# Optimization experiments

Hardware: AMD Instinct MI355X
Metric: run time of the kernel (lower is better)

Reference implementation:

```python
import jax, jax.numpy as jnp
import numpy as np

N, E = 25000, 400000
NF, EF, HNF, HEF = 32, 32, 128, 128
NOUT, EOUT = 32, 32
D_N, D_E = HNF + NF, HEF + EF  # concat dims fed to the GNN layer


def _glorot(key, shape):
    return jax.random.normal(key, shape, jnp.float32) / np.sqrt(shape[0])


def setup_inputs() -> dict:
    key = jax.random.key(0)
    ks = jax.random.split(key, 10)
    return {
        "nf": jax.random.normal(ks[0], (N, NF), jnp.float32),
        "ef": jax.random.normal(ks[1], (E, EF), jnp.float32),
        "src": jax.random.randint(ks[2], (E,), 0, N),
        "dst": jax.random.randint(ks[3], (E,), 0, N),
        # AttnMPNNLayer params: edge model, attention logit model, node model
        "W_edge": _glorot(ks[4], (2 * D_N + D_E, HEF)),
        "b_edge": jnp.zeros((HEF,), jnp.float32),
        "W_attn": _glorot(ks[5], (2 * D_N + D_E, 1)),
        "b_attn": jnp.zeros((1,), jnp.float32),
        "W_node": _glorot(ks[6], (D_N + HEF, HNF)),
        "b_node": jnp.zeros((HNF,), jnp.float32),
        # output heads (MLP with num_neurons=[] -> single Linear)
        "W_nout": _glorot(ks[7], (HNF, NOUT)),
        "b_nout": jnp.zeros((NOUT,), jnp.float32),
        "W_eout": _glorot(ks[8], (HEF, EOUT)),
        "b_eout": jnp.zeros((EOUT,), jnp.float32),
        "n_iters": 3,
    }


def _attn_mpnn_layer(hnf, hef, src, dst, W_edge, b_edge, W_attn, b_attn, W_node, b_node):
    """Attention message passing: gather endpoints, edge MLP + attn logit,
    edge-softmax over incoming edges (per dst node), scatter-aggregate, node MLP."""
    n = hnf.shape[0]
    e_in = jnp.concatenate([hnf[src], hnf[dst], hef], axis=-1)   # [E, 2*D_N + D_E]
    m = jax.nn.relu(e_in @ W_edge + b_edge)                      # [E, HEF] new edge feats
    logit = (e_in @ W_attn + b_attn)[:, 0]                       # [E]
    # numerically stable edge softmax grouped by destination node
    lmax = jax.ops.segment_max(logit, dst, num_segments=n)
    lmax = jnp.where(jnp.isfinite(lmax), lmax, 0.0)              # isolated nodes -> 0
    a = jnp.exp(logit - lmax[dst])
    denom = jax.ops.segment_sum(a, dst, num_segments=n)
    alpha = a / jnp.maximum(denom[dst], 1e-16)
    agg = jax.ops.segment_sum(alpha[:, None] * m, dst, num_segments=n)  # [N, HEF]
    un = jax.nn.relu(jnp.concatenate([hnf, agg], axis=-1) @ W_node + b_node)  # [N, HNF]
    return un, m


def reference(nf, ef, src, dst, W_edge, b_edge, W_attn, b_attn, W_node, b_node,
              W_nout, b_nout, W_eout, b_eout, n_iters):
    hnf = jnp.zeros((nf.shape[0], HNF), nf.dtype)
    hef = jnp.zeros((ef.shape[0], HEF), ef.dtype)
    for _ in range(n_iters):
        hnf = jnp.concatenate([hnf, nf], axis=-1)   # input re-injection
        hef = jnp.concatenate([hef, ef], axis=-1)
        hnf, hef = _attn_mpnn_layer(hnf, hef, src, dst,
                                    W_edge, b_edge, W_attn, b_attn, W_node, b_node)
    unf = hnf @ W_nout + b_nout
    uef = hef @ W_eout + b_eout
    return unf, uef
```

## Files before the change

### kernel.cpp

```cpp
#include <hip/hip_runtime.h>


#define GN 25000
#define GE 400000
#define NODE_BLKS 196
#define EDGE_BLKS 6250
#define HEAD_EBLKS 3125

typedef unsigned short u16;
typedef __attribute__((ext_vector_type(8))) short bf16x8;
typedef __attribute__((ext_vector_type(4))) float f32x4;

__device__ inline float b2f(u16 v) {
  union { unsigned int u; float f; } x; x.u = ((unsigned int)v) << 16; return x.f;
}
__device__ inline u16 f2b(float f) {
  union { float f; unsigned int u; } x; x.f = f;
  unsigned int u = x.u;
  u += 0x7fffu + ((u >> 16) & 1u);
  return (u16)(u >> 16);
}

__global__ void detect_dtype(const void* nf, int* flag) {
  if (blockIdx.x == 0 && threadIdx.x == 0) {
    const u16* p = (const u16*)nf;
    int cnt = 0;
    for (int i = 0; i < 512; i += 2) {
      int e = (p[i] >> 7) & 0xFF;
      if (e >= 0x70 && e <= 0x85) cnt++;
    }
    *flag = (cnt < 128) ? 1 : 0;
  }
}

__global__ void convert_kernel(const void* src, u16* dst, long n, const int* flag) {
  int f32 = *flag;
  long i = (long)blockIdx.x * blockDim.x + threadIdx.x;
  long stride = (long)gridDim.x * blockDim.x;
  for (; i < n; i += stride)
    dst[i] = f32 ? f2b(((const float*)src)[i]) : ((const u16*)src)[i];
}

__global__ void gather_ef(const void* ef, const int* eid, u16* efc, const int* flag) {
  int f32 = *flag;
  long idx = (long)blockIdx.x * blockDim.x + threadIdx.x;
  long ntot = (long)GE * 4;
  if (idx >= ntot) return;
  long j = idx >> 2;
  int g = (int)(idx & 3) * 8;
  long e = eid[j];
  uint4 out;
  if (f32) {
    const float* pf = (const float*)ef + e * 32 + g;
    float4 a = ((const float4*)pf)[0];
    float4 b = ((const float4*)pf)[1];
    unsigned int* ov = (unsigned int*)&out;
    ov[0] = (unsigned int)f2b(a.x) | ((unsigned int)f2b(a.y) << 16);
    ov[1] = (unsigned int)f2b(a.z) | ((unsigned int)f2b(a.w) << 16);
    ov[2] = (unsigned int)f2b(b.x) | ((unsigned int)f2b(b.y) << 16);
    ov[3] = (unsigned int)f2b(b.z) | ((unsigned int)f2b(b.w) << 16);
  } else {
    out = *(const uint4*)((const u16*)ef + e * 32 + g);
  }
  *(uint4*)(efc + j * 32 + g) = out;
}

__global__ void prep_weights(const void* We, const void* Wn, const void* Wa,
                             const void* Won, const void* Woe,
                             const void* be, const void* ba, const void* bn,
                             const void* bno, const void* beo,
                             u16* WeT, u16* WnpT, u16* WnuT, u16* WoN, u16* WoE,
                             u16* Wac, u16* bec, u16* bac, u16* bnc, u16* bnoc, u16* beoc,
                             const int* flag) {
  int f32 = *flag;
  auto ld = [&](const void* p, long i) -> u16 {
    return f32 ? f2b(((const float*)p)[i]) : ((const u16*)p)[i];
  };
  int tid = blockIdx.x * blockDim.x + threadIdx.x;
  int nt = gridDim.x * blockDim.x;
  for (int i = tid; i < 128 * 160; i += nt) { int n = i / 160, k = i % 160; WeT[i] = ld(We, (long)(320 + k) * 128 + n); }
  for (int i = tid; i < 256 * 160; i += nt) {
    int c = i / 160, k = i % 160;
    WnpT[i] = (c < 128) ? ld(We, (long)k * 128 + c) : ld(We, (long)(160 + k) * 128 + (c - 128));
  }
  for (int i = tid; i < 128 * 288; i += nt) { int c = i / 288, k = i % 288; WnuT[i] = ld(Wn, (long)k * 128 + c); }
  for (int i = tid; i < 32 * 128; i += nt) {
    int c = i / 128, k = i % 128;
    WoN[i] = ld(Won, (long)k * 32 + c);
    WoE[i] = ld(Woe, (long)k * 32 + c);
  }
  for (int i = tid; i < 480; i += nt) Wac[i] = ld(Wa, i);
  for (int i = tid; i < 128; i += nt) { bec[i] = ld(be, i); bnc[i] = ld(bn, i); }
  for (int i = tid; i < 32; i += nt) { bnoc[i] = ld(bno, i); beoc[i] = ld(beo, i); }
  if (tid == 0) bac[0] = ld(ba, 0);
}

__global__ void hist_kernel(const int* dst, int* counts, int n) {
  for (int e = blockIdx.x * blockDim.x + threadIdx.x; e < n; e += gridDim.x * blockDim.x)
    atomicAdd(&counts[dst[e]], 1);
}

__global__ __launch_bounds__(1024) void scan_kernel(int* cursor, int* rowptr, int n) {
  __shared__ int part[1024];
  int t = threadIdx.x;
  int per = (n + 1023) / 1024;
  int lo = t * per;
  int hi = lo + per; if (hi > n) hi = n;
  if (lo > n) lo = n;
  int s = 0;
  for (int i = lo; i < hi; ++i) s += cursor[i];
  part[t] = s;
  __syncthreads();
  for (int off = 1; off < 1024; off <<= 1) {
    int v = (t >= off) ? part[t - off] : 0;
    __syncthreads();
    part[t] += v;
    __syncthreads();
  }
  int run = (t > 0) ? part[t - 1] : 0;
  for (int i = lo; i < hi; ++i) {
    int c = cursor[i];
    cursor[i] = run;
    rowptr[i + 1] = run + c;
    run += c;
  }
  if (t == 0) rowptr[0] = 0;
}

__global__ void fill_kernel(const int* src, const int* dst, int* cursor, int* eid,
                            int* srcs, int* dsts, int n) {
  for (int e = blockIdx.x * blockDim.x + threadIdx.x; e < n; e += gridDim.x * blockDim.x) {
    int d = dst[e];
    int p = atomicAdd(&cursor[d], 1);
    eid[p] = e;
    srcs[p] = src[e];
    dsts[p] = d;
  }
}

__global__ __launch_bounds__(256)
void node_proj(const u16* HNF, const u16* nf, const u16* WnpT, const u16* W_attn,
               u16* Xs, u16* Xd, float* as_, float* ad_, int kc0, int nrows) {
  __shared__ union {
    struct { __align__(16) u16 A[128][40]; __align__(16) u16 B[128][40]; } st;
    u16 C[128][130];
  } sm;
  __shared__ float dotbuf[128][2];
  int sel = blockIdx.y, blk = blockIdx.x, tid = threadIdx.x;
  int lane = tid & 63, wv = tid >> 6, wr = wv & 1, wc = wv >> 1;
  const u16* BT = WnpT + sel * 128 * 160;
  u16* OUT = sel ? Xd : Xs;
  float* AOUT = sel ? ad_ : as_;
  const u16* wa = W_attn + sel * 160;
  f32x4 acc[4][4];
  f32x4 zf = {0.f, 0.f, 0.f, 0.f};
  for (int i = 0; i < 4; ++i) for (int j = 0; j < 4; ++j) acc[i][j] = zf;
  float dp = 0.f;
  int arow = tid >> 1, ahalf = (tid & 1) * 16;
  int r0 = blk * 128;
  int ra = r0 + arow;
  uint4 va0 = make_uint4(0, 0, 0, 0), va1 = make_uint4(0, 0, 0, 0), vb0, vb1;
  {
    if (ra < nrows) {
      const uint4* p = (kc0 < 4) ? (const uint4*)(HNF + (size_t)ra * 128 + kc0 * 32 + ahalf)
                                 : (const uint4*)(nf + (size_t)ra * 32 + ahalf);
      va0 = p[0]; va1 = p[1];
    }
    const uint4* pb = (const uint4*)(BT + arow * 160 + kc0 * 32 + ahalf);
    vb0 = pb[0]; vb1 = pb[1];
  }
  for (int kc = kc0; kc < 5; ++kc) {
    *(uint4*)&sm.st.A[arow][ahalf] = va0;
    *(uint4*)&sm.st.A[arow][ahalf + 8] = va1;
    *(uint4*)&sm.st.B[arow][ahalf] = vb0;
    *(uint4*)&sm.st.B[arow][ahalf + 8] = vb1;
    if (kc < 4) {
      int kn = kc + 1;
      va0 = make_uint4(0, 0, 0, 0); va1 = make_uint4(0, 0, 0, 0);
      if (ra < nrows) {
        const uint4* p = (kn < 4) ? (const uint4*)(HNF + (size_t)ra * 128 + kn * 32 + ahalf)
                                  : (const uint4*)(nf + (size_t)ra * 32 + ahalf);
        va0 = p[0]; va1 = p[1];
      }
      const uint4* pb = (const uint4*)(BT + arow * 160 + kn * 32 + ahalf);
      vb0 = pb[0]; vb1 = pb[1];
    }
    __syncthreads();
    {
      float s = 0.f;
      for (int j = 0; j < 16; ++j) s += b2f(sm.st.A[arow][ahalf + j]) * b2f(wa[kc * 32 + ahalf + j]);
      dp += s;
    }
    int q = lane >> 4, l16 = lane & 15;
    bf16x8 af[4], bfr[4];
    for (int i = 0; i < 4; ++i) af[i] = *(const bf16x8*)&sm.st.A[wr * 64 + i * 16 + l16][q * 8];
    for (int j = 0; j < 4; ++j) bfr[j] = *(const bf16x8*)&sm.st.B[wc * 64 + j * 16 + l16][q * 8];
    for (int i = 0; i < 4; ++i)
      for (int j = 0; j < 4; ++j)
        acc[i][j] = __builtin_amdgcn_mfma_f32_16x16x32_bf16(af[i], bfr[j], acc[i][j], 0, 0, 0);
    __syncthreads();
  }
  dotbuf[arow][tid & 1] = dp;
  {
    int q = lane >> 4, l16 = lane & 15;
    for (int i = 0; i < 4; ++i)
      for (int j = 0; j < 4; ++j) {
        int col = wc * 64 + j * 16 + l16;
        for (int rr = 0; rr < 4; ++rr) {
          int row = wr * 64 + i * 16 + q * 4 + rr;
          sm.C[row][col] = f2b(acc[i][j][rr]);
        }
      }
  }
  __syncthreads();
  if (tid < 128) {
    int r = r0 + tid;
    if (r < nrows) AOUT[r] = dotbuf[tid][0] + dotbuf[tid][1];
  }
  {
    int r = tid >> 1, h = (tid & 1) * 64;
    int rg = r0 + r;
    if (rg < nrows) {
      uint4* po = (uint4*)(OUT + (size_t)rg * 128 + h);
      for (int k = 0; k < 8; ++k) {
        unsigned int a0 = *(const unsigned int*)&sm.C[r][h + k * 8];
        unsigned int a1 = *(const unsigned int*)&sm.C[r][h + k * 8 + 2];
        unsigned int a2 = *(const unsigned int*)&sm.C[r][h + k * 8 + 4];
        unsigned int a3 = *(const unsigned int*)&sm.C[r][h + k * 8 + 6];
        po[k] = make_uint4(a0, a1, a2, a3);
      }
    }
  }
}

template <int KC0>
__global__ __launch_bounds__(256, 4)
void edge_fused(u16* HEF, const u16* ef, const u16* WeT, const u16* W_attn,
                const u16* b_edge, const u16* b_attn, const int* srcs, const int* dsts,
                const u16* Xs, const u16* Xd, const float* as_, const float* ad_,
                float* logit) {
  __shared__ union {
    __align__(16) u16 A[2][64][40];
    float C[64][65];
  } sm;
  __shared__ float dotbuf[64];
  int blk = blockIdx.x, tid = threadIdx.x;
  int lane = tid & 63, wv = tid >> 6, wr = wv & 1, wc = wv >> 1;
  int q = lane >> 4, l16 = lane & 15;
  f32x4 acc[2][4];
  f32x4 zf = {0.f, 0.f, 0.f, 0.f};
  for (int i = 0; i < 2; ++i) for (int j = 0; j < 4; ++j) acc[i][j] = zf;
  float dp[2] = {0.f, 0.f};
  long e0 = (long)blk * 64;
  long ea = e0 + (tid >> 2);
  int qp = (tid & 3) * 8;
  const u16* wa = W_attn + 320;

  uint4 va = (KC0 < 4) ? *(const uint4*)(HEF + ea * 128 + KC0 * 32 + qp)
                       : *(const uint4*)(ef + ea * 32 + qp);
  bf16x8 bfp[2][4];
#pragma unroll
  for (int j = 0; j < 4; ++j)
    bfp[KC0 & 1][j] = *(const bf16x8*)(WeT + (size_t)(wc * 64 + j * 16 + l16) * 160 + KC0 * 32 + q * 8);

#pragma unroll
  for (int kc = KC0; kc < 5; ++kc) {
    int buf = kc & 1;
    *(uint4*)&sm.A[buf][tid >> 2][qp] = va;
    if (kc < 4) {
      va = (kc + 1 < 4) ? *(const uint4*)(HEF + ea * 128 + (kc + 1) * 32 + qp)
                        : *(const uint4*)(ef + ea * 32 + qp);
#pragma unroll
      for (int j = 0; j < 4; ++j)
        bfp[(kc + 1) & 1][j] = *(const bf16x8*)(WeT + (size_t)(wc * 64 + j * 16 + l16) * 160 + (kc + 1) * 32 + q * 8);
    }
    __syncthreads();
    bf16x8 af[2];
    for (int i = 0; i < 2; ++i) af[i] = *(const bf16x8*)&sm.A[buf][wr * 32 + i * 16 + l16][q * 8];
    if (wc == 0) {
      bf16x8 wv8 = *(const bf16x8*)&wa[kc * 32 + q * 8];
      float wf[8];
      for (int j = 0; j < 8; ++j) wf[j] = b2f((u16)wv8[j]);
      for (int i = 0; i < 2; ++i)
        for (int j = 0; j < 8; ++j) dp[i] += b2f((u16)af[i][j]) * wf[j];
    }
    for (int i = 0; i < 2; ++i)
      for (int j = 0; j < 4; ++j)
        acc[i][j] = __builtin_amdgcn_mfma_f32_16x16x32_bf16(af[i], bfp[buf][j], acc[i][j], 0, 0, 0);
  }
  if (wc == 0) {
    for (int i = 0; i < 2; ++i) {
      dp[i] += __shfl_xor(dp[i], 16);
      dp[i] += __shfl_xor(dp[i], 32);
    }
    if (q == 0)
      for (int i = 0; i < 2; ++i) dotbuf[wr * 32 + i * 16 + l16] = dp[i];
  }
  int r = tid >> 2, qh = tid & 3;
  long e = e0 + r;
  int s = srcs[e], d = dsts[e];
#pragma unroll
  for (int p = 0; p < 2; ++p) {
    int cb = p * 64 + qh * 16;
    const uint4* ps = (const uint4*)(Xs + (size_t)s * 128 + cb);
    const uint4* pd = (const uint4*)(Xd + (size_t)d * 128 + cb);
    uint4 gs0 = ps[0], gs1 = ps[1], gd0 = pd[0], gd1 = pd[1];
    __syncthreads();
    if (wc == p) {
      for (int i = 0; i < 2; ++i)
        for (int j = 0; j < 4; ++j) {
          int col = j * 16 + l16;
          float bb = b2f(b_edge[p * 64 + col]);
          for (int rr = 0; rr < 4; ++rr)
            sm.C[wr * 32 + i * 16 + q * 4 + rr][col] = acc[i][j][rr] + bb;
        }
    }
    __syncthreads();
    if (p == 0 && tid < 64) {
      long ee = e0 + tid;
      logit[ee] = dotbuf[tid] + as_[srcs[ee]] + ad_[dsts[ee]] + b2f(b_attn[0]);
    }
    unsigned int us[8], ud[8];
    *(uint4*)&us[0] = gs0; *(uint4*)&us[4] = gs1;
    *(uint4*)&ud[0] = gd0; *(uint4*)&ud[4] = gd1;
    unsigned int ov[8];
    for (int w = 0; w < 8; ++w) {
      float c0 = sm.C[r][qh * 16 + 2 * w];
      float c1 = sm.C[r][qh * 16 + 2 * w + 1];
      float v0 = c0 + b2f((u16)(us[w] & 0xffffu)) + b2f((u16)(ud[w] & 0xffffu));
      float v1 = c1 + b2f((u16)(us[w] >> 16)) + b2f((u16)(ud[w] >> 16));
      ov[w] = (unsigned int)f2b(fmaxf(v0, 0.f)) | ((unsigned int)f2b(fmaxf(v1, 0.f)) << 16);
    }
    uint4* po = (uint4*)(HEF + e * 128 + cb);
    po[0] = *(uint4*)&ov[0];
    po[1] = *(uint4*)&ov[4];
  }
}

__global__ __launch_bounds__(256)
void aggregate(const int* rowptr, const float* logit, const u16* M, u16* AGG, int nrows) {
  int gw = (blockIdx.x * blockDim.x + threadIdx.x) >> 6;
  int lane = threadIdx.x & 63;
  if (gw >= nrows) return;
  int beg = rowptr[gw], end = rowptr[gw + 1];
  int sub = lane >> 3, cl = lane & 7;
  float mx = -1e30f;
  for (int j = beg + lane; j < end; j += 64) mx = fmaxf(mx, logit[j]);
  for (int off = 32; off > 0; off >>= 1) mx = fmaxf(mx, __shfl_xor(mx, off));
  float acc[16];
  for (int t = 0; t < 16; ++t) acc[t] = 0.f;
  float denom = 0.f;
  float wc = 0.f;
  uint4 m0c = make_uint4(0, 0, 0, 0), m1c = make_uint4(0, 0, 0, 0);
  {
    int j = beg + sub;
    if (j < end) {
      wc = __expf(logit[j] - mx);
      const uint4* mp = (const uint4*)(M + (size_t)j * 128 + cl * 16);
      m0c = mp[0]; m1c = mp[1];
    }
  }
  for (int j0 = beg; j0 < end; j0 += 8) {
    float wn = 0.f;
    uint4 m0n = make_uint4(0, 0, 0, 0), m1n = make_uint4(0, 0, 0, 0);
    int jn = j0 + 8 + sub;
    if (jn < end) {
      wn = __expf(logit[jn] - mx);
      const uint4* mp = (const uint4*)(M + (size_t)jn * 128 + cl * 16);
      m0n = mp[0]; m1n = mp[1];
    }
    denom += wc;
    const unsigned int* mw0 = (const unsigned int*)&m0c;
    const unsigned int* mw1 = (const unsigned int*)&m1c;
    for (int t = 0; t < 4; ++t) {
      acc[2 * t]     += wc * b2f((u16)(mw0[t] & 0xffffu));
      acc[2 * t + 1] += wc * b2f((u16)(mw0[t] >> 16));
      acc[8 + 2 * t]     += wc * b2f((u16)(mw1[t] & 0xffffu));
      acc[8 + 2 * t + 1] += wc * b2f((u16)(mw1[t] >> 16));
    }
    wc = wn; m0c = m0n; m1c = m1n;
  }
  denom += __shfl_xor(denom, 8);
  denom += __shfl_xor(denom, 16);
  denom += __shfl_xor(denom, 32);
  for (int t = 0; t < 16; ++t) {
    acc[t] += __shfl_xor(acc[t], 8);
    acc[t] += __shfl_xor(acc[t], 16);
    acc[t] += __shfl_xor(acc[t], 32);
  }
  float inv = 1.0f / fmaxf(denom, 1e-16f);
  if (sub == 0) {
    unsigned int ov[8];
    for (int t = 0; t < 8; ++t)
      ov[t] = (unsigned int)f2b(acc[2 * t] * inv) | ((unsigned int)f2b(acc[2 * t + 1] * inv) << 16);
    uint4* po = (uint4*)(AGG + (size_t)gw * 128 + cl * 16);
    po[0] = *(uint4*)&ov[0];
    po[1] = *(uint4*)&ov[4];
  }
}

__global__ __launch_bounds__(256)
void node_update(u16* HNF, const u16* nf, const u16* AGG, const u16* WnuT,
                 const u16* b_node, int kc0, int nrows) {
  __shared__ union {
    struct { __align__(16) u16 A[128][40]; __align__(16) u16 B[128][40]; } st;
    u16 C[128][130];
  } sm;
  int blk = blockIdx.x, tid = threadIdx.x;
  int lane = tid & 63, wv = tid >> 6, wr = wv & 1, wc = wv >> 1;
  f32x4 acc[4][4];
  f32x4 zf = {0.f, 0.f, 0.f, 0.f};
  for (int i = 0; i < 4; ++i) for (int j = 0; j < 4; ++j) acc[i][j] = zf;
  int arow = tid >> 1, ahalf = (tid & 1) * 16;
  int r0 = blk * 128;
  int ra = r0 + arow;
  auto asrc = [&](int kc) -> const u16* {
    if (kc < 4) return HNF + (size_t)ra * 128 + kc * 32 + ahalf;
    if (kc == 4) return nf + (size_t)ra * 32 + ahalf;
    return AGG + (size_t)ra * 128 + (kc - 5) * 32 + ahalf;
  };
  uint4 va0 = make_uint4(0, 0, 0, 0), va1 = make_uint4(0, 0, 0, 0), vb0, vb1;
  {
    if (ra < nrows) {
      const uint4* p = (const uint4*)asrc(kc0);
      va0 = p[0]; va1 = p[1];
    }
    const uint4* pb = (const uint4*)(WnuT + arow * 288 + kc0 * 32 + ahalf);
    vb0 = pb[0]; vb1 = pb[1];
  }
  for (int kc = kc0; kc < 9; ++kc) {
    *(uint4*)&sm.st.A[arow][ahalf] = va0;
    *(uint4*)&sm.st.A[arow][ahalf + 8] = va1;
    *(uint4*)&sm.st.B[arow][ahalf] = vb0;
    *(uint4*)&sm.st.B[arow][ahalf + 8] = vb1;
    if (kc < 8) {
      int kn = kc + 1;
      va0 = make_uint4(0, 0, 0, 0); va1 = make_uint4(0, 0, 0, 0);
      if (ra < nrows) {
        const uint4* p = (const uint4*)asrc(kn);
        va0 = p[0]; va1 = p[1];
      }
      const uint4* pb = (const uint4*)(WnuT + arow * 288 + kn * 32 + ahalf);
      vb0 = pb[0]; vb1 = pb[1];
    }
    __syncthreads();
    int q = lane >> 4, l16 = lane & 15;
    bf16x8 af[4], bfr[4];
    for (int i = 0; i < 4; ++i) af[i] = *(const bf16x8*)&sm.st.A[wr * 64 + i * 16 + l16][q * 8];
    for (int j = 0; j < 4; ++j) bfr[j] = *(const bf16x8*)&sm.st.B[wc * 64 + j * 16 + l16][q * 8];
    for (int i = 0; i < 4; ++i)
      for (int j = 0; j < 4; ++j)
        acc[i][j] = __builtin_amdgcn_mfma_f32_16x16x32_bf16(af[i], bfr[j], acc[i][j], 0, 0, 0);
    __syncthreads();
  }
  int q = lane >> 4, l16 = lane & 15;
  for (int i = 0; i < 4; ++i)
    for (int j = 0; j < 4; ++j) {
      int col = wc * 64 + j * 16 + l16;
      float bb = b2f(b_node[col]);
      for (int rr = 0; rr < 4; ++rr) {
        int row = wr * 64 + i * 16 + q * 4 + rr;
        sm.C[row][col] = f2b(fmaxf(acc[i][j][rr] + bb, 0.f));
      }
    }
  __syncthreads();
  {
    int r = tid >> 1, h = (tid & 1) * 64;
    int rg = r0 + r;
    if (rg < nrows) {
      uint4* po = (uint4*)(HNF + (size_t)rg * 128 + h);
      for (int k = 0; k < 8; ++k) {
        unsigned int a0 = *(const unsigned int*)&sm.C[r][h + k * 8];
        unsigned int a1 = *(const unsigned int*)&sm.C[r][h + k * 8 + 2];
        unsigned int a2 = *(const unsigned int*)&sm.C[r][h + k * 8 + 4];
        unsigned int a3 = *(const unsigned int*)&sm.C[r][h + k * 8 + 6];
        po[k] = make_uint4(a0, a1, a2, a3);
      }
    }
  }
}

__global__ __launch_bounds__(256)
void head_kernel(const u16* IN, const u16* WT, const u16* bias, float* OUT, long R,
                 const int* remap) {
  __shared__ __align__(16) u16 Asm[128][40];
  __shared__ __align__(16) u16 Bsm[32][40];
  int blk = blockIdx.x, tid = threadIdx.x;
  int lane = tid & 63, wv = tid >> 6;
  f32x4 acc[2][2];
  f32x4 zf = {0.f, 0.f, 0.f, 0.f};
  for (int i = 0; i < 2; ++i) for (int j = 0; j < 2; ++j) acc[i][j] = zf;
  int arow = tid >> 1, ahalf = (tid & 1) * 16;
  long r0 = (long)blk * 128;
  long ra = r0 + arow;
  uint4 va0 = make_uint4(0, 0, 0, 0), va1 = make_uint4(0, 0, 0, 0);
  uint4 vb0 = make_uint4(0, 0, 0, 0), vb1 = make_uint4(0, 0, 0, 0);
  {
    if (ra < R) {
      const uint4* p = (const uint4*)(IN + ra * 128 + 0 * 32 + ahalf);
      va0 = p[0]; va1 = p[1];
    }
    if (tid < 64) {
      const uint4* p = (const uint4*)(WT + arow * 128 + 0 * 32 + ahalf);
      vb0 = p[0]; vb1 = p[1];
    }
  }
  for (int kc = 0; kc < 4; ++kc) {
    *(uint4*)&Asm[arow][ahalf] = va0;
    *(uint4*)&Asm[arow][ahalf + 8] = va1;
    if (tid < 64) {
      *(uint4*)&Bsm[arow][ahalf] = vb0;
      *(uint4*)&Bsm[arow][ahalf + 8] = vb1;
    }
    if (kc < 3) {
      int kn = kc + 1;
      va0 = make_uint4(0, 0, 0, 0); va1 = make_uint4(0, 0, 0, 0);
      if (ra < R) {
        const uint4* p = (const uint4*)(IN + ra * 128 + kn * 32 + ahalf);
        va0 = p[0]; va1 = p[1];
      }
      if (tid < 64) {
        const uint4* p = (const uint4*)(WT + arow * 128 + kn * 32 + ahalf);
        vb0 = p[0]; vb1 = p[1];
      }
    }
    __syncthreads();
    int q = lane >> 4, l16 = lane & 15;
    bf16x8 af[2], bfr[2];
    for (int i = 0; i < 2; ++i) af[i] = *(const bf16x8*)&Asm[wv * 32 + i * 16 + l16][q * 8];
    for (int j = 0; j < 2; ++j) bfr[j] = *(const bf16x8*)&Bsm[j * 16 + l16][q * 8];
    for (int i = 0; i < 2; ++i)
      for (int j = 0; j < 2; ++j)
        acc[i][j] = __builtin_amdgcn_mfma_f32_16x16x32_bf16(af[i], bfr[j], acc[i][j], 0, 0, 0);
    __syncthreads();
  }
  int q = lane >> 4, l16 = lane & 15;
  for (int i = 0; i < 2; ++i)
    for (int rr = 0; rr < 4; ++rr) {
      long r = r0 + wv * 32 + i * 16 + q * 4 + rr;
      if (r < R) {
        long ro = remap ? (long)remap[r] : r;
        for (int j = 0; j < 2; ++j) {
          int col = j * 16 + l16;
          OUT[ro * 32 + col] = acc[i][j][rr] + b2f(bias[col]);
        }
      }
    }
}

extern "C" void kernel_launch(void* const* d_in, const int* in_sizes, int n_in,
                              void* d_out, int out_size, void* d_ws, size_t ws_size,
                              hipStream_t stream) {
  const size_t REQUIRED = 160000000;
  if (ws_size < REQUIRED) return;

  const void* nf_r = d_in[0];
  const void* ef_r = d_in[1];
  const int* src = (const int*)d_in[2];
  const int* dst = (const int*)d_in[3];

  char* ws = (char*)d_ws;
  auto alloc = [&](size_t bytes) {
    char* p = ws;
    ws += (bytes + 255) & ~(size_t)255;
    return p;
  };
  u16* HEF = (u16*)alloc((size_t)GE * 128 * 2);
  u16* HNF = (u16*)alloc((size_t)GN * 128 * 2);
  u16* Xs = (u16*)alloc((size_t)GN * 128 * 2);
  u16* Xd = (u16*)alloc((size_t)GN * 128 * 2);
  float* as_ = (float*)alloc((size_t)GN * 4);
  float* ad_ = (float*)alloc((size_t)GN * 4);
  float* logit = (float*)alloc((size_t)GE * 4);
  int* rowptr = (int*)alloc((size_t)(GN + 1) * 4);
  int* cursor = (int*)alloc((size_t)GN * 4);
  int* eid = (int*)alloc((size_t)GE * 4);
  int* srcs = (int*)alloc((size_t)GE * 4);
  int* dsts = (int*)alloc((size_t)GE * 4);
  u16* WeT = (u16*)alloc(128 * 160 * 2);
  u16* WnpT = (u16*)alloc(256 * 160 * 2);
  u16* WnuT = (u16*)alloc(128 * 288 * 2);
  u16* WoN = (u16*)alloc(32 * 128 * 2);
  u16* WoE = (u16*)alloc(32 * 128 * 2);
  u16* nfc = (u16*)alloc((size_t)GN * 32 * 2);
  u16* efc = (u16*)alloc((size_t)GE * 32 * 2);
  u16* bec = (u16*)alloc(128 * 2);
  u16* Wac = (u16*)alloc(480 * 2);
  u16* bac = (u16*)alloc(2);
  u16* bnc = (u16*)alloc(128 * 2);
  u16* bnoc = (u16*)alloc(32 * 2);
  u16* beoc = (u16*)alloc(32 * 2);
  int* dflag = (int*)alloc(4);
  u16* AGG = Xs;

  detect_dtype<<<1, 64, 0, stream>>>(nf_r, dflag);
  hipMemsetAsync(cursor, 0, (size_t)GN * 4, stream);
  hist_kernel<<<1563, 256, 0, stream>>>(dst, cursor, GE);
  scan_kernel<<<1, 1024, 0, stream>>>(cursor, rowptr, GN);
  fill_kernel<<<1563, 256, 0, stream>>>(src, dst, cursor, eid, srcs, dsts, GE);

  convert_kernel<<<784, 256, 0, stream>>>(nf_r, nfc, (long)GN * 32, dflag);
  gather_ef<<<6250, 256, 0, stream>>>(ef_r, eid, efc, dflag);
  prep_weights<<<128, 256, 0, stream>>>(d_in[4], d_in[8], d_in[6], d_in[10], d_in[12],
                                        d_in[5], d_in[7], d_in[9], d_in[11], d_in[13],
                                        WeT, WnpT, WnuT, WoN, WoE,
                                        Wac, bec, bac, bnc, bnoc, beoc, dflag);

  for (int iter = 0; iter < 3; ++iter) {
    int kc0 = (iter == 0) ? 4 : 0;
    dim3 npgrid(NODE_BLKS, 2);
    node_proj<<<npgrid, 256, 0, stream>>>(HNF, nfc, WnpT, Wac, Xs, Xd, as_, ad_, kc0, GN);
    if (iter == 0)
      edge_fused<4><<<EDGE_BLKS, 256, 0, stream>>>(HEF, efc, WeT, Wac, bec, bac, srcs, dsts,
                                                   Xs, Xd, as_, ad_, logit);
    else
      edge_fused<0><<<EDGE_BLKS, 256, 0, stream>>>(HEF, efc, WeT, Wac, bec, bac, srcs, dsts,
                                                   Xs, Xd, as_, ad_, logit);
    aggregate<<<(GN + 3) / 4, 256, 0, stream>>>(rowptr, logit, HEF, AGG, GN);
    node_update<<<NODE_BLKS, 256, 0, stream>>>(HNF, nfc, AGG, WnuT, bnc, kc0, GN);
  }

  float* out_nf = (float*)d_out;
  float* out_ef = (float*)d_out + (size_t)GN * 32;
  head_kernel<<<NODE_BLKS, 256, 0, stream>>>(HNF, WoN, bnoc, out_nf, GN, nullptr);
  head_kernel<<<HEAD_EBLKS, 256, 0, stream>>>(HEF, WoE, beoc, out_ef, GE, eid);
}
```

Measured before the change: 603.6 us.

## Fuse output heads into final edge_fused and node_update kernels

The separate head_kernel launches are removed. In the last iteration, edge_fused stages its relu output tile in shared memory and runs the 128->32 edge head with MFMA, scattering results through eid. node_update likewise applies the node head from its shared C tile. This avoids re-reading HEF and HNF from global memory and saves two launches, but adds shared memory (which may lower occupancy) and per-wave weight loads from global memory in the last iteration.

```diff
diff --git a/kernel.cpp b/kernel.cpp
--- a/kernel.cpp
+++ b/kernel.cpp
@@ -5,7 +5,6 @@
 #define GE 400000
 #define NODE_BLKS 196
 #define EDGE_BLKS 6250
-#define HEAD_EBLKS 3125
 
 typedef unsigned short u16;
 typedef __attribute__((ext_vector_type(8))) short bf16x8;
@@ -233,17 +232,19 @@
   }
 }
 
-template <int KC0>
+template <int KC0, int LAST>
 __global__ __launch_bounds__(256, 4)
 void edge_fused(u16* HEF, const u16* ef, const u16* WeT, const u16* W_attn,
                 const u16* b_edge, const u16* b_attn, const int* srcs, const int* dsts,
                 const u16* Xs, const u16* Xd, const float* as_, const float* ad_,
-                float* logit) {
+                float* logit, const u16* WoE, const u16* b_eout, const int* eid,
+                float* out_ef) {
   __shared__ union {
     __align__(16) u16 A[2][64][40];
     float C[64][65];
   } sm;
   __shared__ float dotbuf[64];
+  __shared__ __align__(16) u16 Mt[LAST ? 64 : 1][136];
   int blk = blockIdx.x, tid = threadIdx.x;
   int lane = tid & 63, wv = tid >> 6, wr = wv & 1, wc = wv >> 1;
   int q = lane >> 4, l16 = lane & 15;
@@ -331,9 +332,32 @@
       float v1 = c1 + b2f((u16)(us[w] >> 16)) + b2f((u16)(ud[w] >> 16));
       ov[w] = (unsigned int)f2b(fmaxf(v0, 0.f)) | ((unsigned int)f2b(fmaxf(v1, 0.f)) << 16);
     }
+    if (LAST) {
+      *(uint4*)&Mt[r][cb] = *(uint4*)&ov[0];
+      *(uint4*)&Mt[r][cb + 8] = *(uint4*)&ov[4];
+    }
     uint4* po = (uint4*)(HEF + e * 128 + cb);
     po[0] = *(uint4*)&ov[0];
     po[1] = *(uint4*)&ov[4];
+  }
+  if (LAST) {
+    __syncthreads();
+    f32x4 ha0 = zf, ha1 = zf;
+#pragma unroll
+    for (int kc2 = 0; kc2 < 4; ++kc2) {
+      bf16x8 af2 = *(const bf16x8*)&Mt[wv * 16 + l16][kc2 * 32 + q * 8];
+      bf16x8 b0 = *(const bf16x8*)(WoE + (size_t)l16 * 128 + kc2 * 32 + q * 8);
+      bf16x8 b1 = *(const bf16x8*)(WoE + (size_t)(16 + l16) * 128 + kc2 * 32 + q * 8);
+      ha0 = __builtin_amdgcn_mfma_f32_16x16x32_bf16(af2, b0, ha0, 0, 0, 0);
+      ha1 = __builtin_amdgcn_mfma_f32_16x16x32_bf16(af2, b1, ha1, 0, 0, 0);
+    }
+    float bb0 = b2f(b_eout[l16]), bb1 = b2f(b_eout[16 + l16]);
+    for (int rr = 0; rr < 4; ++rr) {
+      long ee = e0 + wv * 16 + q * 4 + rr;
+      long ro = eid[ee];
+      out_ef[ro * 32 + l16] = ha0[rr] + bb0;
+      out_ef[ro * 32 + 16 + l16] = ha1[rr] + bb1;
+    }
   }
 }
 
@@ -399,9 +423,11 @@
   }
 }
 
+template <int LAST>
 __global__ __launch_bounds__(256)
 void node_update(u16* HNF, const u16* nf, const u16* AGG, const u16* WnuT,
-                 const u16* b_node, int kc0, int nrows) {
+                 const u16* b_node, int kc0, int nrows,
+                 const u16* WoN, const u16* b_nout, float* out_nf) {
   __shared__ union {
     struct { __align__(16) u16 A[128][40]; __align__(16) u16 B[128][40]; } st;
     u16 C[128][130];
@@ -478,74 +504,32 @@
       }
     }
   }
-}
-
-__global__ __launch_bounds__(256)
-void head_kernel(const u16* IN, const u16* WT, const u16* bias, float* OUT, long R,
-                 const int* remap) {
-  __shared__ __align__(16) u16 Asm[128][40];
-  __shared__ __align__(16) u16 Bsm[32][40];
-  int blk = blockIdx.x, tid = threadIdx.x;
-  int lane = tid & 63, wv = tid >> 6;
-  f32x4 acc[2][2];
-  f32x4 zf = {0.f, 0.f, 0.f, 0.f};
-  for (int i = 0; i < 2; ++i) for (int j = 0; j < 2; ++j) acc[i][j] = zf;
-  int arow = tid >> 1, ahalf = (tid & 1) * 16;
-  long r0 = (long)blk * 128;
-  long ra = r0 + arow;
-  uint4 va0 = make_uint4(0, 0, 0, 0), va1 = make_uint4(0, 0, 0, 0);
-  uint4 vb0 = make_uint4(0, 0, 0, 0), vb1 = make_uint4(0, 0, 0, 0);
-  {
-    if (ra < R) {
-      const uint4* p = (const uint4*)(IN + ra * 128 + 0 * 32 + ahalf);
-      va0 = p[0]; va1 = p[1];
-    }
-    if (tid < 64) {
-      const uint4* p = (const uint4*)(WT + arow * 128 + 0 * 32 + ahalf);
-      vb0 = p[0]; vb1 = p[1];
-    }
-  }
-  for (int kc = 0; kc < 4; ++kc) {
-    *(uint4*)&Asm[arow][ahalf] = va0;
-    *(uint4*)&Asm[arow][ahalf + 8] = va1;
-    if (tid < 64) {
-      *(uint4*)&Bsm[arow][ahalf] = vb0;
-      *(uint4*)&Bsm[arow][ahalf + 8] = vb1;
-    }
-    if (kc < 3) {
-      int kn = kc + 1;
-      va0 = make_uint4(0, 0, 0, 0); va1 = make_uint4(0, 0, 0, 0);
-      if (ra < R) {
-        const uint4* p = (const uint4*)(IN + ra * 128 + kn * 32 + ahalf);
-        va0 = p[0]; va1 = p[1];
-      }
-      if (tid < 64) {
-        const uint4* p = (const uint4*)(WT + arow * 128 + kn * 32 + ahalf);
-        vb0 = p[0]; vb1 = p[1];
-      }
-    }
-    __syncthreads();
-    int q = lane >> 4, l16 = lane & 15;
-    bf16x8 af[2], bfr[2];
-    for (int i = 0; i < 2; ++i) af[i] = *(const bf16x8*)&Asm[wv * 32 + i * 16 + l16][q * 8];
-    for (int j = 0; j < 2; ++j) bfr[j] = *(const bf16x8*)&Bsm[j * 16 + l16][q * 8];
+  if (LAST) {
+    f32x4 ha[2][2];
+    for (int i = 0; i < 2; ++i) for (int j = 0; j < 2; ++j) ha[i][j] = zf;
+#pragma unroll
+    for (int kc2 = 0; kc2 < 4; ++kc2) {
+      bf16x8 af2[2], bf2[2];
+      for (int i = 0; i < 2; ++i) {
+        unsigned int* ap = (unsigned int*)&af2[i];
+        int row = wv * 32 + i * 16 + l16;
+        for (int w = 0; w < 4; ++w)
+          ap[w] = *(const unsigned int*)&sm.C[row][kc2 * 32 + q * 8 + 2 * w];
+      }
+      for (int j = 0; j < 2; ++j)
+        bf2[j] = *(const bf16x8*)(WoN + (size_t)(j * 16 + l16) * 128 + kc2 * 32 + q * 8);
+      for (int i = 0; i < 2; ++i)
+        for (int j = 0; j < 2; ++j)
+          ha[i][j] = __builtin_amdgcn_mfma_f32_16x16x32_bf16(af2[i], bf2[j], ha[i][j], 0, 0, 0);
+    }
     for (int i = 0; i < 2; ++i)
-      for (int j = 0; j < 2; ++j)
-        acc[i][j] = __builtin_amdgcn_mfma_f32_16x16x32_bf16(af[i], bfr[j], acc[i][j], 0, 0, 0);
-    __syncthreads();
-  }
-  int q = lane >> 4, l16 = lane & 15;
-  for (int i = 0; i < 2; ++i)
-    for (int rr = 0; rr < 4; ++rr) {
-      long r = r0 + wv * 32 + i * 16 + q * 4 + rr;
-      if (r < R) {
-        long ro = remap ? (long)remap[r] : r;
-        for (int j = 0; j < 2; ++j) {
-          int col = j * 16 + l16;
-          OUT[ro * 32 + col] = acc[i][j][rr] + b2f(bias[col]);
-        }
-      }
-    }
+      for (int rr = 0; rr < 4; ++rr) {
+        int rowg = r0 + wv * 32 + i * 16 + q * 4 + rr;
+        if (rowg < nrows)
+          for (int j = 0; j < 2; ++j)
+            out_nf[(size_t)rowg * 32 + j * 16 + l16] = ha[i][j][rr] + b2f(b_nout[j * 16 + l16]);
+      }
+  }
 }
 
 extern "C" void kernel_launch(void* const* d_in, const int* in_sizes, int n_in,
@@ -593,6 +577,9 @@
   int* dflag = (int*)alloc(4);
   u16* AGG = Xs;
 
+  float* out_nf = (float*)d_out;
+  float* out_ef = (float*)d_out + (size_t)GN * 32;
+
   detect_dtype<<<1, 64, 0, stream>>>(nf_r, dflag);
   hipMemsetAsync(cursor, 0, (size_t)GN * 4, stream);
   hist_kernel<<<1563, 256, 0, stream>>>(dst, cursor, GE);
@@ -611,17 +598,20 @@
     dim3 npgrid(NODE_BLKS, 2);
     node_proj<<<npgrid, 256, 0, stream>>>(HNF, nfc, WnpT, Wac, Xs, Xd, as_, ad_, kc0, GN);
     if (iter == 0)
-      edge_fused<4><<<EDGE_BLKS, 256, 0, stream>>>(HEF, efc, WeT, Wac, bec, bac, srcs, dsts,
-                                                   Xs, Xd, as_, ad_, logit);
+      edge_fused<4, 0><<<EDGE_BLKS, 256, 0, stream>>>(HEF, efc, WeT, Wac, bec, bac, srcs, dsts,
+                                                      Xs, Xd, as_, ad_, logit, WoE, beoc, eid, out_ef);
+    else if (iter == 1)
+      edge_fused<0, 0><<<EDGE_BLKS, 256, 0, stream>>>(HEF, efc, WeT, Wac, bec, bac, srcs, dsts,
+                                                      Xs, Xd, as_, ad_, logit, WoE, beoc, eid, out_ef);
     else
-      edge_fused<0><<<EDGE_BLKS, 256, 0, stream>>>(HEF, efc, WeT, Wac, bec, bac, srcs, dsts,
-                                                   Xs, Xd, as_, ad_, logit);
+      edge_fused<0, 1><<<EDGE_BLKS, 256, 0, stream>>>(HEF, efc, WeT, Wac, bec, bac, srcs, dsts,
+                                                      Xs, Xd, as_, ad_, logit, WoE, beoc, eid, out_ef);
     aggregate<<<(GN + 3) / 4, 256, 0, stream>>>(rowptr, logit, HEF, AGG, GN);
-    node_update<<<NODE_BLKS, 256, 0, stream>>>(HNF, nfc, AGG, WnuT, bnc, kc0, GN);
-  }
-
-  float* out_nf = (float*)d_out;
-  float* out_ef = (float*)d_out + (size_t)GN * 32;
-  head_kernel<<<NODE_BLKS, 256, 0, stream>>>(HNF, WoN, bnoc, out_nf, GN, nullptr);
-  head_kernel<<<HEAD_EBLKS, 256, 0, stream>>>(HEF, WoE, beoc, out_ef, GE, eid);
-}
+    if (iter < 2)
+      node_update<0><<<NODE_BLKS, 256, 0, stream>>>(HNF, nfc, AGG, WnuT, bnc, kc0, GN,
+                                                    WoN, bnoc, out_nf);
+    else
+      node_update<1><<<NODE_BLKS, 256, 0, stream>>>(HNF, nfc, AGG, WnuT, bnc, kc0, GN,
+                                                    WoN, bnoc, out_nf);
+  }
+}
```

After: 593.5 us. Within noise of the previous version (-1.7%).
